# Performance work log

Hardware: AMD Instinct MI355X
Metric: run time of the kernel (lower is better)

## Reference

```python
import jax, jax.numpy as jnp
import numpy as np

N_EMBD = 1024
N_HEAD = 16
SEQ_LEN = 2048
BATCH = 4
ROPE_THETA = 10000.0


def _rope_tables(T, hd, dtype=jnp.float32):
    freqs = 1.0 / (ROPE_THETA ** (jnp.arange(0, hd, 2, dtype=jnp.float32) / hd))
    t = jnp.arange(T, dtype=jnp.float32)
    ang = jnp.outer(t, freqs)  # [T, hd//2]
    return jnp.cos(ang).astype(dtype), jnp.sin(ang).astype(dtype)


def _apply_rope(x, cos, sin):
    # x: [B,H,T,hd]; cos/sin: [T, hd//2]
    hd = x.shape[-1]
    x1, x2 = x[..., : hd // 2], x[..., hd // 2 :]
    c = cos[None, None, : x.shape[2], :]
    s = sin[None, None, : x.shape[2], :]
    return jnp.concatenate([x1 * c - x2 * s, x2 * c + x1 * s], axis=-1)


def _rms_norm(x):
    eps = jnp.finfo(x.dtype).eps
    return x * jax.lax.rsqrt(jnp.mean(jnp.square(x), axis=-1, keepdims=True) + eps)


def setup_inputs() -> dict:
    key = jax.random.key(0)
    k1, k2, k3, k4 = jax.random.split(key, 4)
    C = N_EMBD
    x = jax.random.normal(k1, (BATCH, SEQ_LEN, C), dtype=jnp.float32)
    w_attn = jax.random.normal(k2, (C, 3 * C), dtype=jnp.float32) * (1.0 / np.sqrt(C))
    w_proj = jax.random.normal(k3, (C, C), dtype=jnp.float32) * (1.0 / np.sqrt(C))
    val_embed = jax.random.normal(k4, (SEQ_LEN, C), dtype=jnp.float32) * 0.02
    return {"x": x, "w_attn": w_attn, "w_proj": w_proj, "val_embed": val_embed}


def reference(x, w_attn, w_proj, val_embed):
    B, T, C = x.shape
    H = N_HEAD
    hd = C // H

    qkv = x @ w_attn  # [B,T,3C]
    q, k, v = jnp.split(qkv, 3, axis=-1)
    v = v + val_embed[:T]

    def to_heads(t):
        return t.reshape(B, T, H, hd).transpose(0, 2, 1, 3)  # [B,H,T,hd]

    q, k, v = to_heads(q), to_heads(k), to_heads(v)

    cos, sin = _rope_tables(T, hd, x.dtype)
    q = _rms_norm(_apply_rope(q, cos, sin))
    k = _rms_norm(_apply_rope(k, cos, sin))

    scale = 1.0 / np.sqrt(hd)
    scores = jnp.einsum("bhqd,bhkd->bhqk", q, k) * scale  # [B,H,T,T]
    causal = jnp.tril(jnp.ones((T, T), dtype=bool))
    scores = jnp.where(causal[None, None], scores, jnp.finfo(scores.dtype).min)
    attn = jax.nn.softmax(scores, axis=-1)
    y = jnp.einsum("bhqk,bhkd->bhqd", attn, v)  # [B,H,T,hd]
    y = y.transpose(0, 2, 1, 3).reshape(B, T, C)
    return y @ w_proj
```

## Files before the change

kernel.cpp:

```cpp
#include <hip/hip_runtime.h>
#include <float.h>
#include <math.h>

#define BB 4
#define TT 2048
#define CC 1024
#define HH 16
#define HD 64
#define C3 3072

typedef __bf16 bf16;
typedef __bf16 bf16x8 __attribute__((ext_vector_type(8)));
typedef __bf16 bf16x4 __attribute__((ext_vector_type(4)));
typedef float f32x4 __attribute__((ext_vector_type(4)));
typedef float f32x16 __attribute__((ext_vector_type(16)));
typedef unsigned int uint32x4 __attribute__((ext_vector_type(4)));

#define QSCALE 0.18033688f

__device__ __forceinline__ void gload16(const void* g, void* l) {
    __builtin_amdgcn_global_load_lds(
        (const __attribute__((address_space(1))) void*)g,
        (__attribute__((address_space(3))) void*)l, 16, 0, 0);
}

__global__ __launch_bounds__(256) void rope_table_k(float* __restrict__ tab) {
    int idx = blockIdx.x * 256 + threadIdx.x;
    if (idx >= TT * 32) return;
    int t = idx >> 5;
    int j = idx & 31;
    float freq = powf(10000.0f, -((float)(2 * j)) / 64.0f);
    float ang = (float)t * freq;
    tab[idx] = cosf(ang);
    tab[TT * 32 + idx] = sinf(ang);
}

__global__ __launch_bounds__(256) void cvt_f2b_k(const float* __restrict__ in,
                                                 bf16* __restrict__ out, int n8) {
    int i = blockIdx.x * 256 + threadIdx.x;
    if (i >= n8) return;
    const float4* p = (const float4*)(in + (size_t)i * 8);
    float4 a = p[0], b = p[1];
    bf16x8 o;
    o[0] = (bf16)a.x; o[1] = (bf16)a.y; o[2] = (bf16)a.z; o[3] = (bf16)a.w;
    o[4] = (bf16)b.x; o[5] = (bf16)b.y; o[6] = (bf16)b.z; o[7] = (bf16)b.w;
    *(bf16x8*)(out + (size_t)i * 8) = o;
}

__global__ __launch_bounds__(256) void transW_k(const float* __restrict__ in,
                                                bf16* __restrict__ out, int K, int N) {
    __shared__ bf16 tile[64][72];
    int n0 = blockIdx.x * 64, k0 = blockIdx.y * 64;
    int t = threadIdx.x;
    int r = t >> 2, c4 = (t & 3) * 16;
    const float4* src = (const float4*)(in + (size_t)(k0 + r) * N + n0 + c4);
    #pragma unroll
    for (int j = 0; j < 4; ++j) {
        float4 v = src[j];
        tile[r][c4 + 4 * j + 0] = (bf16)v.x; tile[r][c4 + 4 * j + 1] = (bf16)v.y;
        tile[r][c4 + 4 * j + 2] = (bf16)v.z; tile[r][c4 + 4 * j + 3] = (bf16)v.w;
    }
    __syncthreads();
    bf16x8 o0, o1;
    #pragma unroll
    for (int j = 0; j < 8; ++j) o0[j] = tile[c4 + j][r];
    #pragma unroll
    for (int j = 0; j < 8; ++j) o1[j] = tile[c4 + 8 + j][r];
    *(bf16x8*)(out + (size_t)(n0 + r) * K + k0 + c4) = o0;
    *(bf16x8*)(out + (size_t)(n0 + r) * K + k0 + c4 + 8) = o1;
}

__global__ __launch_bounds__(512, 1) void gemm256_k(const bf16* __restrict__ A,
                                                    const bf16* __restrict__ BT,
                                                    bf16* __restrict__ Qh,
                                                    bf16* __restrict__ Kh,
                                                    bf16* __restrict__ Vh,
                                                    int M, int N, int K) {
    extern __shared__ bf16 smem[];
    const int ATILE = 256 * 64;
    const int BTILE = 192 * 64;
    const int tid = threadIdx.x;
    const int w = tid >> 6, lane = tid & 63;
    const int wm = w >> 2, wn = w & 3;
    const int nwg = (int)gridDim.x;
    const int cpx = nwg >> 3;
    const int flat = (int)blockIdx.x;
    const int wg = (flat & 7) * cpx + (flat >> 3);
    const int gx = N / 192;
    const int n0 = (wg % gx) * 192;
    const int m0 = (wg / gx) * 256;

    const int srow = lane >> 3;
    const int schunk = (lane & 7) ^ srow;
    const int xorL = (lane & 7) << 3;
    const int KT = K >> 6;

    f32x4 acc[8][3];
    #pragma unroll
    for (int i = 0; i < 8; ++i)
        #pragma unroll
        for (int j = 0; j < 3; ++j) acc[i][j] = {0.f, 0.f, 0.f, 0.f};

    auto stage = [&](int kt, bf16* Abuf, bf16* Bbuf) {
        const int k0 = kt * 64;
        #pragma unroll
        for (int ri = 0; ri < 7; ++ri) {
            int row = ri * 64 + w * 8;
            if (row < 256) {
                gload16(A + (size_t)(m0 + row + srow) * K + k0 + schunk * 8,
                        Abuf + row * 64);
            } else {
                int rb = row - 256;
                gload16(BT + (size_t)(n0 + rb + srow) * K + k0 + schunk * 8,
                        Bbuf + rb * 64);
            }
        }
    };

    stage(0, smem, smem + ATILE);
    __syncthreads();

    for (int kt = 0; kt < KT; ++kt) {
        const int buf = kt & 1;
        if (kt + 1 < KT) {
            bf16* base = smem + (buf ^ 1) * (ATILE + BTILE);
            stage(kt + 1, base, base + ATILE);
        }
        const bf16* Al = smem + buf * (ATILE + BTILE);
        const bf16* Bl = Al + ATILE;
        #pragma unroll
        for (int kh = 0; kh < 2; ++kh) {
            const int off = (kh * 32 + (lane >> 4) * 8) ^ xorL;
            bf16x8 aF[8], bF[3];
            #pragma unroll
            for (int i = 0; i < 8; ++i)
                aF[i] = *(const bf16x8*)&Al[(wm * 128 + i * 16 + (lane & 15)) * 64 + off];
            #pragma unroll
            for (int j = 0; j < 3; ++j)
                bF[j] = *(const bf16x8*)&Bl[(wn * 48 + j * 16 + (lane & 15)) * 64 + off];
            __builtin_amdgcn_s_setprio(1);
            #pragma unroll
            for (int i = 0; i < 8; ++i)
                #pragma unroll
                for (int j = 0; j < 3; ++j)
                    acc[i][j] = __builtin_amdgcn_mfma_f32_16x16x32_bf16(
                        aF[i], bF[j], acc[i][j], 0, 0, 0);
            __builtin_amdgcn_s_setprio(0);
        }
        __syncthreads();
    }

    const int ncb = n0 + wn * 48;
    #pragma unroll
    for (int j = 0; j < 3; ++j) {
        const int ncbj = ncb + j * 16;
        const int region = ncbj >> 10;
        const int hj = (ncbj & 1023) >> 6;
        const int cj = (ncbj & 63) + (lane & 15);
        bf16* dst = (region == 0) ? Qh : ((region == 1) ? Kh : Vh);
        #pragma unroll
        for (int i = 0; i < 8; ++i)
            #pragma unroll
            for (int r = 0; r < 4; ++r) {
                int m = m0 + wm * 128 + i * 16 + 4 * (lane >> 4) + r;
                int b = m >> 11, t = m & (TT - 1);
                dst[((size_t)(b * HH + hj) * TT + t) * HD + cj] = (bf16)acc[i][j][r];
            }
    }
}

__global__ __launch_bounds__(256) void gemm_bt_k(const bf16* __restrict__ A,
                                                 const bf16* __restrict__ BT,
                                                 float* __restrict__ C,
                                                 int M, int N, int K) {
    __shared__ bf16 Al[128 * 64];
    __shared__ bf16 Bl[128 * 64];
    const int tid = threadIdx.x;
    const int w = tid >> 6, lane = tid & 63;
    const int flat = (int)blockIdx.x;
    const int xcd = flat & 7;
    const int local = flat >> 3;
    const int lr = local >> 3, lc = local & 7;
    const int m0 = (xcd * 8 + lr) * 128;
    const int n0 = lc * 128;
    const int wrow = (w >> 1) * 64, wcol = (w & 1) * 64;
    const int srow = lane >> 3;
    const int selem = (((lane & 7) ^ srow) << 3);
    const int xorL = (lane & 7) << 3;

    const f32x4 fz = {0.f, 0.f, 0.f, 0.f};
    f32x4 acc[4][4];
    #pragma unroll
    for (int i = 0; i < 4; ++i)
        #pragma unroll
        for (int j = 0; j < 4; ++j) acc[i][j] = fz;

    for (int k0 = 0; k0 < K; k0 += 64) {
        __syncthreads();
        #pragma unroll
        for (int jj = 0; jj < 4; ++jj) {
            int c = w * 4 + jj;
            int row = c * 8 + srow;
            gload16(A + (size_t)(m0 + row) * K + k0 + selem, &Al[c * 512]);
            gload16(BT + (size_t)(n0 + row) * K + k0 + selem, &Bl[c * 512]);
        }
        __syncthreads();
        #pragma unroll
        for (int kh = 0; kh < 2; ++kh) {
            const int off = (kh * 32 + (lane >> 4) * 8) ^ xorL;
            bf16x8 aF[4], bF[4];
            #pragma unroll
            for (int i = 0; i < 4; ++i) {
                aF[i] = *(const bf16x8*)&Al[(wrow + i * 16 + (lane & 15)) * 64 + off];
                bF[i] = *(const bf16x8*)&Bl[(wcol + i * 16 + (lane & 15)) * 64 + off];
            }
            #pragma unroll
            for (int i = 0; i < 4; ++i)
                #pragma unroll
                for (int j = 0; j < 4; ++j)
                    acc[i][j] = __builtin_amdgcn_mfma_f32_16x16x32_bf16(
                        aF[i], bF[j], acc[i][j], 0, 0, 0);
        }
    }

    #pragma unroll
    for (int i = 0; i < 4; ++i)
        #pragma unroll
        for (int r = 0; r < 4; ++r) {
            size_t rowm = (size_t)(m0 + wrow + i * 16 + 4 * (lane >> 4) + r);
            #pragma unroll
            for (int j = 0; j < 4; ++j)
                C[rowm * N + n0 + wcol + j * 16 + (lane & 15)] = acc[i][j][r];
        }
}

__global__ __launch_bounds__(256) void rope_rms_k(bf16* __restrict__ Qh,
                                                  bf16* __restrict__ Kh,
                                                  const bf16* __restrict__ Vh,
                                                  bf16* __restrict__ Vt,
                                                  const float* __restrict__ emb,
                                                  const float* __restrict__ tab) {
    __shared__ bf16 tile[64][72];
    const int t0 = blockIdx.x * 64;
    const int bh = blockIdx.y;
    const int h = bh & (HH - 1);
    const int w = threadIdx.x >> 6, lane = threadIdx.x & 63;
    const int j = lane & 31;
    #pragma unroll 4
    for (int i = 0; i < 16; ++i) {
        const int tl = w * 16 + i;
        const int t = t0 + tl;
        const size_t base = ((size_t)bh * TT + t) * HD + lane;
        const float cs = tab[t * 32 + j];
        const float sn = tab[TT * 32 + t * 32 + j];
        float q = (float)Qh[base], k = (float)Kh[base], v = (float)Vh[base];
        float qp = __shfl_xor(q, 32, 64), kp = __shfl_xor(k, 32, 64);
        float rq = (lane < 32) ? q * cs - qp * sn : q * cs + qp * sn;
        float rk = (lane < 32) ? k * cs - kp * sn : k * cs + kp * sn;
        float sq = rq * rq, sk = rk * rk;
        #pragma unroll
        for (int off = 1; off < 64; off <<= 1) {
            sq += __shfl_xor(sq, off, 64);
            sk += __shfl_xor(sk, off, 64);
        }
        rq *= rsqrtf(sq * (1.0f / 64.0f) + 1.1920929e-07f);
        rk *= rsqrtf(sk * (1.0f / 64.0f) + 1.1920929e-07f);
        Qh[base] = (bf16)(rq * QSCALE);
        Kh[base] = (bf16)rk;
        tile[tl][lane] = (bf16)(v + emb[(size_t)t * CC + h * HD + lane]);
    }
    __syncthreads();
    const int tt = threadIdx.x;
    const int r = tt >> 2, c4 = (tt & 3) * 16;
    bf16x8 o0, o1;
    #pragma unroll
    for (int jj = 0; jj < 8; ++jj) o0[jj] = tile[c4 + jj][r];
    #pragma unroll
    for (int jj = 0; jj < 8; ++jj) o1[jj] = tile[c4 + 8 + jj][r];
    bf16* out = Vt + (size_t)bh * HD * TT;
    *(bf16x8*)(out + (size_t)r * TT + t0 + c4) = o0;
    *(bf16x8*)(out + (size_t)r * TT + t0 + c4 + 8) = o1;
}

__global__ __launch_bounds__(512) void attn_k(const bf16* __restrict__ Qh,
                                              const bf16* __restrict__ Kh,
                                              const bf16* __restrict__ Vt,
                                              bf16* __restrict__ Y) {
    const int flat = (int)blockIdx.y * 8 + (int)blockIdx.x;
    const int slot = flat >> 3;
    const int bh = (flat & 7) * 8 + (slot & 7);
    const int u = slot >> 3;
    const int qb = (u < 4) ? (7 - u) : (u - 4);
    const int b = bh >> 4, h = bh & 15;
    const int tid = threadIdx.x, w = tid >> 6, lane = tid & 63;
    const int hi = lane >> 5, q31 = lane & 31;
    const int wq0 = qb * 256 + w * 32;
    const int qg = wq0 + q31;
    const int xr = q31 & 7;

    __shared__ bf16 Kl[3][64 * 64];
    __shared__ bf16 Vl[3][64 * 64];

    const bf16* Kbase = Kh + (size_t)bh * TT * HD;
    const bf16* Vbase = Vt + (size_t)bh * HD * TT;

    bf16x8 qF[4];
    {
        const bf16* qp = Qh + (size_t)bh * TT * HD + (size_t)qg * HD + hi * 8;
        #pragma unroll
        for (int ds = 0; ds < 4; ++ds) qF[ds] = *(const bf16x8*)(qp + ds * 16);
    }

    f32x16 accY[2];
    #pragma unroll
    for (int i = 0; i < 16; ++i) { accY[0][i] = 0.f; accY[1][i] = 0.f; }
    float mR = -INFINITY, lR = 0.f;

    const int srow = lane >> 3;
    const int schunk = (lane & 7) ^ srow;
    const int ktN = 4 * qb + 4;

    {
        int r0 = w * 8 + srow;
        gload16(Kbase + (size_t)r0 * HD + schunk * 8, &Kl[0][w * 512]);
        gload16(Vbase + (size_t)r0 * TT + schunk * 8, &Vl[0][w * 512]);
        gload16(Kbase + (size_t)(64 + r0) * HD + schunk * 8, &Kl[1][w * 512]);
        gload16(Vbase + (size_t)r0 * TT + 64 + schunk * 8, &Vl[1][w * 512]);
    }
    asm volatile("s_waitcnt vmcnt(2)" ::: "memory");
    __builtin_amdgcn_s_barrier();
    __builtin_amdgcn_sched_barrier(0);

    int bufC = 0, bufS = 2;
    for (int kt = 0; kt < ktN; ++kt) {
        if (kt + 2 < ktN) {
            int trow = (kt + 2) * 64 + w * 8 + srow;
            int drow = w * 8 + srow;
            gload16(Kbase + (size_t)trow * HD + schunk * 8, &Kl[bufS][w * 512]);
            gload16(Vbase + (size_t)drow * TT + (kt + 2) * 64 + schunk * 8,
                    &Vl[bufS][w * 512]);
        }
        if (kt * 64 <= wq0 + 31) {
            const bf16* KL = &Kl[bufC][0];
            const bf16* VL = &Vl[bufC][0];
            f32x16 sa[2];
            #pragma unroll
            for (int i = 0; i < 16; ++i) { sa[0][i] = 0.f; sa[1][i] = 0.f; }
            __builtin_amdgcn_s_setprio(1);
            #pragma unroll
            for (int ds = 0; ds < 4; ++ds) {
                int cc = ds * 2 + hi;
                bf16x8 k0 = *(const bf16x8*)&KL[q31 * 64 + ((cc ^ xr) * 8)];
                bf16x8 k1 = *(const bf16x8*)&KL[(32 + q31) * 64 + ((cc ^ xr) * 8)];
                sa[0] = __builtin_amdgcn_mfma_f32_32x32x16_bf16(k0, qF[ds], sa[0], 0, 0, 0);
                sa[1] = __builtin_amdgcn_mfma_f32_32x32x16_bf16(k1, qF[ds], sa[1], 0, 0, 0);
            }
            __builtin_amdgcn_s_setprio(0);
            if (kt * 64 + 63 > wq0) {
                #pragma unroll
                for (int kb = 0; kb < 2; ++kb)
                    #pragma unroll
                    for (int r = 0; r < 16; ++r) {
                        int k = kt * 64 + kb * 32 + (r & 3) + 8 * (r >> 2) + 4 * hi;
                        if (k > qg) sa[kb][r] = -1e30f;
                    }
            }
            float mx = -1e30f;
            #pragma unroll
            for (int r = 0; r < 16; ++r)
                mx = fmaxf(fmaxf(sa[0][r], sa[1][r]), mx);
            mx = fmaxf(mx, __shfl_xor(mx, 32, 64));
            if (!__all(mx - mR <= 12.0f)) {
                float mnew = fmaxf(mR, mx);
                float alpha = __builtin_amdgcn_exp2f(mR - mnew);
                #pragma unroll
                for (int i = 0; i < 16; ++i) { accY[0][i] *= alpha; accY[1][i] *= alpha; }
                lR *= alpha;
                mR = mnew;
            }
            float sum0 = 0.f, sum1 = 0.f;
            #pragma unroll
            for (int r = 0; r < 16; ++r) {
                float p0 = __builtin_amdgcn_exp2f(sa[0][r] - mR);
                float p1 = __builtin_amdgcn_exp2f(sa[1][r] - mR);
                sa[0][r] = p0; sa[1][r] = p1;
                sum0 += p0; sum1 += p1;
            }
            float sum = sum0 + sum1;
            sum += __shfl_xor(sum, 32, 64);
            lR += sum;
            unsigned int wds[2][8];
            #pragma unroll
            for (int kb = 0; kb < 2; ++kb)
                #pragma unroll
                for (int jj = 0; jj < 8; ++jj) {
                    bf16x8 tmp;
                    tmp[0] = (bf16)sa[kb][2 * jj];
                    tmp[1] = (bf16)sa[kb][2 * jj + 1];
                    wds[kb][jj] = *(unsigned int*)&tmp;
                }
            bf16x8 pF[4];
            #pragma unroll
            for (int ks = 0; ks < 4; ++ks) {
                const int kb = ks >> 1, s = ks & 1;
                unsigned int w0 = wds[kb][4 * s + 0], w1 = wds[kb][4 * s + 1];
                unsigned int w2 = wds[kb][4 * s + 2], w3 = wds[kb][4 * s + 3];
                unsigned int t0 = hi ? w0 : w2, t1 = hi ? w1 : w3;
                unsigned int r0 = (unsigned int)__shfl_xor((int)t0, 32, 64);
                unsigned int r1 = (unsigned int)__shfl_xor((int)t1, 32, 64);
                uint32x4 fw;
                fw[0] = hi ? r0 : w0; fw[1] = hi ? r1 : w1;
                fw[2] = hi ? w2 : r0; fw[3] = hi ? w3 : r1;
                pF[ks] = *(bf16x8*)&fw;
            }
            __builtin_amdgcn_s_setprio(1);
            #pragma unroll
            for (int cd = 0; cd < 2; ++cd) {
                const int rowD = cd * 32 + q31;
                #pragma unroll
                for (int ks = 0; ks < 4; ++ks) {
                    int cc = ks * 2 + hi;
                    bf16x8 vA = *(const bf16x8*)&VL[rowD * 64 + ((cc ^ xr) * 8)];
                    accY[cd] = __builtin_amdgcn_mfma_f32_32x32x16_bf16(
                        vA, pF[ks], accY[cd], 0, 0, 0);
                }
            }
            __builtin_amdgcn_s_setprio(0);
        }
        if (kt + 1 < ktN) {
            if (kt + 2 < ktN) {
                asm volatile("s_waitcnt vmcnt(2)" ::: "memory");
            } else {
                asm volatile("s_waitcnt vmcnt(0)" ::: "memory");
            }
            __builtin_amdgcn_s_barrier();
            __builtin_amdgcn_sched_barrier(0);
        }
        bufC = (bufC == 2) ? 0 : bufC + 1;
        bufS = (bufS == 2) ? 0 : bufS + 1;
    }

    float inv = 1.0f / lR;
    bf16* yp = Y + ((size_t)(b * TT + qg)) * CC + h * HD;
    #pragma unroll
    for (int cd = 0; cd < 2; ++cd)
        #pragma unroll
        for (int g = 0; g < 4; ++g) {
            int d0 = cd * 32 + 8 * g + 4 * hi;
            bf16x4 o;
            o[0] = (bf16)(accY[cd][4 * g + 0] * inv);
            o[1] = (bf16)(accY[cd][4 * g + 1] * inv);
            o[2] = (bf16)(accY[cd][4 * g + 2] * inv);
            o[3] = (bf16)(accY[cd][4 * g + 3] * inv);
            *(bf16x4*)(yp + d0) = o;
        }
}

extern "C" void kernel_launch(void* const* d_in, const int* in_sizes, int n_in,
                              void* d_out, int out_size, void* d_ws, size_t ws_size,
                              hipStream_t stream) {
    const float* x         = (const float*)d_in[0];
    const float* w_attn    = (const float*)d_in[1];
    const float* w_proj    = (const float*)d_in[2];
    const float* val_embed = (const float*)d_in[3];
    float* out = (float*)d_out;

    bf16* xb  = (bf16*)d_ws;
    bf16* waT = xb + (size_t)8192 * 1024;
    bf16* wpT = waT + (size_t)3072 * 1024;
    bf16* Qh  = wpT + (size_t)1024 * 1024;
    bf16* Kh  = Qh + (size_t)64 * 2048 * 64;
    bf16* Vh  = Kh + (size_t)64 * 2048 * 64;
    bf16* Vt  = Vh + (size_t)64 * 2048 * 64;
    bf16* Yb  = Vt + (size_t)64 * 2048 * 64;
    float* tab = (float*)(Yb + (size_t)64 * 2048 * 64);

    hipFuncSetAttribute((const void*)gemm256_k,
                        hipFuncAttributeMaxDynamicSharedMemorySize, 114688);

    rope_table_k<<<dim3((TT * 32 + 255) / 256), dim3(256), 0, stream>>>(tab);
    cvt_f2b_k<<<dim3(8192 * 1024 / 8 / 256), dim3(256), 0, stream>>>(x, xb, 8192 * 1024 / 8);
    transW_k<<<dim3(3072 / 64, 1024 / 64), dim3(256), 0, stream>>>(w_attn, waT, 1024, 3072);
    transW_k<<<dim3(1024 / 64, 1024 / 64), dim3(256), 0, stream>>>(w_proj, wpT, 1024, 1024);
    gemm256_k<<<dim3((8192 / 256) * (3072 / 192)), dim3(512), 114688, stream>>>(
        xb, waT, Qh, Kh, Vh, 8192, 3072, 1024);
    rope_rms_k<<<dim3(TT / 64, BB * HH), dim3(256), 0, stream>>>(
        Qh, Kh, Vh, Vt, val_embed, tab);
    attn_k<<<dim3(8, BB * HH), dim3(512), 0, stream>>>(Qh, Kh, Vt, Yb);
    gemm_bt_k<<<dim3(512), dim3(256), 0, stream>>>(
        Yb, wpT, out, 8192, 1024, 1024);
}
```

Before: 189.1 us.

## Stage 128-key K/V tiles with double buffering in attention kernel

Changes the attention kernel's K/V staging from triple-buffered 64-key tiles to double-buffered 128-key tiles in dynamic shared memory, with an inner loop over two 64-key sub-tiles. This halves the number of block-wide barriers and wait points per query block. The prefetch distance drops from two tiles to one, and each step now waits for all outstanding loads. Shared memory grows to 64 KB per block, which may reduce occupancy and expose more load latency.

```diff
diff --git a/kernel.cpp b/kernel.cpp
--- a/kernel.cpp
+++ b/kernel.cpp
@@ -286,6 +286,9 @@
                                               const bf16* __restrict__ Kh,
                                               const bf16* __restrict__ Vt,
                                               bf16* __restrict__ Y) {
+    extern __shared__ bf16 asmem[];
+    bf16* KlB = asmem;
+    bf16* VlB = asmem + 16384;
     const int flat = (int)blockIdx.y * 8 + (int)blockIdx.x;
     const int slot = flat >> 3;
     const int bh = (flat & 7) * 8 + (slot & 7);
@@ -298,9 +301,6 @@
     const int qg = wq0 + q31;
     const int xr = q31 & 7;
 
-    __shared__ bf16 Kl[3][64 * 64];
-    __shared__ bf16 Vl[3][64 * 64];
-
     const bf16* Kbase = Kh + (size_t)bh * TT * HD;
     const bf16* Vbase = Vt + (size_t)bh * HD * TT;
 
@@ -318,31 +318,36 @@
 
     const int srow = lane >> 3;
     const int schunk = (lane & 7) ^ srow;
-    const int ktN = 4 * qb + 4;
-
-    {
-        int r0 = w * 8 + srow;
-        gload16(Kbase + (size_t)r0 * HD + schunk * 8, &Kl[0][w * 512]);
-        gload16(Vbase + (size_t)r0 * TT + schunk * 8, &Vl[0][w * 512]);
-        gload16(Kbase + (size_t)(64 + r0) * HD + schunk * 8, &Kl[1][w * 512]);
-        gload16(Vbase + (size_t)r0 * TT + 64 + schunk * 8, &Vl[1][w * 512]);
-    }
-    asm volatile("s_waitcnt vmcnt(2)" ::: "memory");
+    const int vsr = lane >> 4;
+    const int ktN = 2 * qb + 2;
+
+    auto stageKV = [&](int kt, int buf) {
+        const int kc0 = kt * 128;
+        #pragma unroll
+        for (int jj = 0; jj < 2; ++jj) {
+            int lr = w * 16 + jj * 8;
+            gload16(Kbase + (size_t)(kc0 + lr + srow) * HD + schunk * 8,
+                    KlB + buf * 8192 + lr * 64);
+            int vr = w * 8 + jj * 4;
+            int vrow = vr + vsr;
+            gload16(Vbase + (size_t)vrow * TT + kc0 + (((lane & 15) ^ (vrow & 7)) * 8),
+                    VlB + buf * 8192 + vr * 128);
+        }
+    };
+
+    stageKV(0, 0);
+    asm volatile("s_waitcnt vmcnt(0)" ::: "memory");
     __builtin_amdgcn_s_barrier();
     __builtin_amdgcn_sched_barrier(0);
 
-    int bufC = 0, bufS = 2;
     for (int kt = 0; kt < ktN; ++kt) {
-        if (kt + 2 < ktN) {
-            int trow = (kt + 2) * 64 + w * 8 + srow;
-            int drow = w * 8 + srow;
-            gload16(Kbase + (size_t)trow * HD + schunk * 8, &Kl[bufS][w * 512]);
-            gload16(Vbase + (size_t)drow * TT + (kt + 2) * 64 + schunk * 8,
-                    &Vl[bufS][w * 512]);
-        }
-        if (kt * 64 <= wq0 + 31) {
-            const bf16* KL = &Kl[bufC][0];
-            const bf16* VL = &Vl[bufC][0];
+        const int buf = kt & 1;
+        if (kt + 1 < ktN) stageKV(kt + 1, buf ^ 1);
+        const bf16* KL = KlB + buf * 8192;
+        const bf16* VL = VlB + buf * 8192;
+        #pragma unroll
+        for (int s = 0; s < 2; ++s) {
+            if (kt * 128 + s * 64 > wq0 + 31) break;
             f32x16 sa[2];
             #pragma unroll
             for (int i = 0; i < 16; ++i) { sa[0][i] = 0.f; sa[1][i] = 0.f; }
@@ -350,18 +355,18 @@
             #pragma unroll
             for (int ds = 0; ds < 4; ++ds) {
                 int cc = ds * 2 + hi;
-                bf16x8 k0 = *(const bf16x8*)&KL[q31 * 64 + ((cc ^ xr) * 8)];
-                bf16x8 k1 = *(const bf16x8*)&KL[(32 + q31) * 64 + ((cc ^ xr) * 8)];
+                bf16x8 k0 = *(const bf16x8*)&KL[(s * 64 + q31) * 64 + ((cc ^ xr) * 8)];
+                bf16x8 k1 = *(const bf16x8*)&KL[(s * 64 + 32 + q31) * 64 + ((cc ^ xr) * 8)];
                 sa[0] = __builtin_amdgcn_mfma_f32_32x32x16_bf16(k0, qF[ds], sa[0], 0, 0, 0);
                 sa[1] = __builtin_amdgcn_mfma_f32_32x32x16_bf16(k1, qF[ds], sa[1], 0, 0, 0);
             }
             __builtin_amdgcn_s_setprio(0);
-            if (kt * 64 + 63 > wq0) {
+            if (kt * 128 + s * 64 + 63 > wq0) {
                 #pragma unroll
                 for (int kb = 0; kb < 2; ++kb)
                     #pragma unroll
                     for (int r = 0; r < 16; ++r) {
-                        int k = kt * 64 + kb * 32 + (r & 3) + 8 * (r >> 2) + 4 * hi;
+                        int k = kt * 128 + s * 64 + kb * 32 + (r & 3) + 8 * (r >> 2) + 4 * hi;
                         if (k > qg) sa[kb][r] = -1e30f;
                     }
             }
@@ -402,9 +407,9 @@
             bf16x8 pF[4];
             #pragma unroll
             for (int ks = 0; ks < 4; ++ks) {
-                const int kb = ks >> 1, s = ks & 1;
-                unsigned int w0 = wds[kb][4 * s + 0], w1 = wds[kb][4 * s + 1];
-                unsigned int w2 = wds[kb][4 * s + 2], w3 = wds[kb][4 * s + 3];
+                const int kb = ks >> 1, ss = ks & 1;
+                unsigned int w0 = wds[kb][4 * ss + 0], w1 = wds[kb][4 * ss + 1];
+                unsigned int w2 = wds[kb][4 * ss + 2], w3 = wds[kb][4 * ss + 3];
                 unsigned int t0 = hi ? w0 : w2, t1 = hi ? w1 : w3;
                 unsigned int r0 = (unsigned int)__shfl_xor((int)t0, 32, 64);
                 unsigned int r1 = (unsigned int)__shfl_xor((int)t1, 32, 64);
@@ -419,8 +424,8 @@
                 const int rowD = cd * 32 + q31;
                 #pragma unroll
                 for (int ks = 0; ks < 4; ++ks) {
-                    int cc = ks * 2 + hi;
-                    bf16x8 vA = *(const bf16x8*)&VL[rowD * 64 + ((cc ^ xr) * 8)];
+                    int cc = s * 8 + ks * 2 + hi;
+                    bf16x8 vA = *(const bf16x8*)&VL[rowD * 128 + ((cc ^ xr) * 8)];
                     accY[cd] = __builtin_amdgcn_mfma_f32_32x32x16_bf16(
                         vA, pF[ks], accY[cd], 0, 0, 0);
                 }
@@ -428,16 +433,10 @@
             __builtin_amdgcn_s_setprio(0);
         }
         if (kt + 1 < ktN) {
-            if (kt + 2 < ktN) {
-                asm volatile("s_waitcnt vmcnt(2)" ::: "memory");
-            } else {
-                asm volatile("s_waitcnt vmcnt(0)" ::: "memory");
-            }
+            asm volatile("s_waitcnt vmcnt(0)" ::: "memory");
             __builtin_amdgcn_s_barrier();
             __builtin_amdgcn_sched_barrier(0);
         }
-        bufC = (bufC == 2) ? 0 : bufC + 1;
-        bufS = (bufS == 2) ? 0 : bufS + 1;
     }
 
     float inv = 1.0f / lR;
@@ -477,6 +476,8 @@
 
     hipFuncSetAttribute((const void*)gemm256_k,
                         hipFuncAttributeMaxDynamicSharedMemorySize, 114688);
+    hipFuncSetAttribute((const void*)attn_k,
+                        hipFuncAttributeMaxDynamicSharedMemorySize, 65536);
 
     rope_table_k<<<dim3((TT * 32 + 255) / 256), dim3(256), 0, stream>>>(tab);
     cvt_f2b_k<<<dim3(8192 * 1024 / 8 / 256), dim3(256), 0, stream>>>(x, xb, 8192 * 1024 / 8);
@@ -486,7 +487,7 @@
         xb, waT, Qh, Kh, Vh, 8192, 3072, 1024);
     rope_rms_k<<<dim3(TT / 64, BB * HH), dim3(256), 0, stream>>>(
         Qh, Kh, Vh, Vt, val_embed, tab);
-    attn_k<<<dim3(8, BB * HH), dim3(512), 0, stream>>>(Qh, Kh, Vt, Yb);
+    attn_k<<<dim3(8, BB * HH), dim3(512), 65536, stream>>>(Qh, Kh, Vt, Yb);
     gemm_bt_k<<<dim3(512), dim3(256), 0, stream>>>(
         Yb, wpT, out, 8192, 1024, 1024);
 }
```

New measurement: 181.3 us, median of 2. -4.1%, faster.
